# Kernel tuning notes

Measured on AMD Instinct MI355X. Metric: run time of the kernel, lower is better.

## Reference

```python
import jax, jax.numpy as jnp
import numpy as np

N, D, H, O = 2048, 128, 256, 1  # batch, input_dim, hidden_dim, output_dim
LN_EPS = 1e-5


def setup_inputs() -> dict:
    key = jax.random.key(0)
    ks = jax.random.split(key, 10)
    s = lambda fan_in: 1.0 / np.sqrt(fan_in)
    return {
        "array": jax.random.normal(ks[0], (N, D), dtype=jnp.float32),
        # per-feature Linear(1, H) stacked: weight [D, H], bias [D, H]
        "W_in": jax.random.uniform(ks[1], (D, H), jnp.float32, -1.0, 1.0),
        "b_in": jax.random.uniform(ks[2], (D, H), jnp.float32, -1.0, 1.0),
        # FactorAttentionLayer (width D): W: Linear(D, D), V: Linear(D, 1), LayerNorm(D)
        "Wf": jax.random.uniform(ks[3], (D, D), jnp.float32, -s(D), s(D)),
        "bf": jax.random.uniform(ks[4], (D,), jnp.float32, -s(D), s(D)),
        "Vf": jax.random.uniform(ks[5], (D,), jnp.float32, -s(D), s(D)),
        "bv": jnp.zeros((), jnp.float32),
        "ln_g": jnp.ones((D,), jnp.float32),
        "ln_b": jnp.zeros((D,), jnp.float32),
        # fc_hidden: Linear(D*H, H); fc_output: Linear(H, O)  (stored as [in, out])
        "Wh": jax.random.uniform(ks[6], (D * H, H), jnp.float32, -s(D * H), s(D * H)),
        "bh": jax.random.uniform(ks[7], (H,), jnp.float32, -s(D * H), s(D * H)),
        "Wo": jax.random.uniform(ks[8], (H, O), jnp.float32, -s(H), s(H)),
        "bo": jax.random.uniform(ks[9], (O,), jnp.float32, -s(H), s(H)),
    }


def reference(array, W_in, b_in, Wf, bf, Vf, bv, ln_g, ln_b, Wh, bh, Wo, bo):
    # Fused per-feature Linear(1,H)+ReLU: [n, D, H]
    p = jax.nn.relu(array[:, :, None] * W_in[None] + b_in[None])
    # permute(0, 2, 1) -> [n, H, D]
    x = jnp.transpose(p, (0, 2, 1))
    # FactorAttention: tanh-linear, softmax over axis 1 (the H axis), residual mul, LayerNorm over D
    u = jnp.tanh(jnp.einsum('nhd,de->nhe', x, Wf) + bf)          # [n, H, D]
    scores = jnp.einsum('nhd,d->nh', u, Vf) + bv                  # [n, H]
    attn = jax.nn.softmax(scores, axis=1)[:, :, None]             # [n, H, 1]
    y = x + x * attn                                              # [n, H, D]
    mu = jnp.mean(y, axis=-1, keepdims=True)
    var = jnp.mean((y - mu) ** 2, axis=-1, keepdims=True)
    y = (y - mu) * jax.lax.rsqrt(var + LN_EPS) * ln_g + ln_b
    # flatten [n, H*D] and MLP head (dropout = identity in eval)
    xx = y.reshape(y.shape[0], -1)
    h = jax.nn.relu(xx @ Wh + bh)
    return h @ Wo + bo
```

## Files before the change

### kernel.cpp

```cpp
#include <hip/hip_runtime.h>

#define NB 2048
#define DD 128
#define HH 256
#define KF 32768
#define LN_EPS 1e-5f

typedef __attribute__((ext_vector_type(8))) short short8;
typedef __attribute__((ext_vector_type(4))) float float4_t;

__device__ __forceinline__ unsigned short f2bf(float f) {
    unsigned int u = __builtin_bit_cast(unsigned int, f);
    u += 0x7fffu + ((u >> 16) & 1u);
    return (unsigned short)(u >> 16);
}

__device__ __forceinline__ void gl2lds16(const void* g, void* l) {
    __builtin_amdgcn_global_load_lds(
        (const __attribute__((address_space(1))) unsigned int*)g,
        (__attribute__((address_space(3))) unsigned int*)l, 16, 0, 0);
}

__global__ void prep_b(const float* __restrict__ Wh, unsigned short* __restrict__ WhbT) {
    __shared__ unsigned short tile[64][65];
    int kb = blockIdx.x;
    int jb = blockIdx.y;
    int t = threadIdx.x;
    int c = t & 63, r4 = t >> 6;
    int kap0 = kb * 64;
    int d  = kap0 >> 8;
    int h0 = kap0 & 255;
    for (int rr = r4; rr < 64; rr += 4) {
        int k = (h0 + rr) * 128 + d;
        tile[rr][c] = f2bf(Wh[(long)k * 256 + jb * 64 + c]);
    }
    __syncthreads();
    for (int rr = r4; rr < 64; rr += 4) {
        WhbT[(long)(jb * 64 + rr) * KF + kap0 + c] = tile[c][rr];
    }
}

__global__ void zgen(const float* __restrict__ arr, const float* __restrict__ Win,
                     const float* __restrict__ bin, const float* __restrict__ g,
                     const float* __restrict__ beta, unsigned short* __restrict__ Z) {
    __shared__ float a_s[4][128];
    __shared__ float g_s[128], b_s[128];
    int t = threadIdx.x;
    int n0 = blockIdx.x * 4;
    if (t < 128) { g_s[t] = g[t]; b_s[t] = beta[t]; }
    for (int i = t; i < 512; i += 256) a_s[i >> 7][i & 127] = arr[n0 * 128 + i];
    __syncthreads();
    int h = t;
    float sum[4] = {0.f, 0.f, 0.f, 0.f}, ssq[4] = {0.f, 0.f, 0.f, 0.f};
    for (int d = 0; d < 128; ++d) {
        float w = Win[d * 256 + h];
        float bb = bin[d * 256 + h];
#pragma unroll
        for (int q = 0; q < 4; ++q) {
            float x = fmaxf(fmaf(a_s[q][d], w, bb), 0.f);
            sum[q] += x; ssq[q] += x * x;
        }
    }
    float mu[4], rs[4];
#pragma unroll
    for (int q = 0; q < 4; ++q) {
        mu[q] = sum[q] * (1.f / 128.f);
        float var = fmaxf(ssq[q] * (1.f / 128.f) - mu[q] * mu[q], 0.f);
        rs[q] = rsqrtf(var + LN_EPS);
    }
    for (int d = 0; d < 128; ++d) {
        float w = Win[d * 256 + h];
        float bb = bin[d * 256 + h];
        float gg = g_s[d], be = b_s[d];
#pragma unroll
        for (int q = 0; q < 4; ++q) {
            float x = fmaxf(fmaf(a_s[q][d], w, bb), 0.f);
            float zv = fmaf((x - mu[q]) * rs[q], gg, be);
            Z[(long)(n0 + q) * KF + d * 256 + h] = f2bf(zv);
        }
    }
}

#define BM 128
#define BN 128
#define BK 32
#define KSPLIT 16
#define KSL (KF / KSPLIT)

__global__ __launch_bounds__(256, 2) void gemm_k(
        const unsigned short* __restrict__ A,
        const unsigned short* __restrict__ Bt,
        float* __restrict__ Cp) {
    __shared__ unsigned short As[BM * BK];
    __shared__ unsigned short Bs[BN * BK];
    int bid = blockIdx.x;
    int ks = bid >> 5;
    int mt = (bid >> 1) & 15;
    int nt = bid & 1;
    int m0 = mt * BM, n0 = nt * BN, k0 = ks * KSL;
    int t = threadIdx.x;
    int lane = t & 63, wave = t >> 6;
    int wm = (wave >> 1) * 64, wn = (wave & 1) * 64;
    int fr = lane & 15;
    int fk = (lane >> 4) * 8;

    float4_t acc[4][4] = {};

    const unsigned short* Aab = A + (long)m0 * KF + k0;
    const unsigned short* Bab = Bt + (long)n0 * KF + k0;
    int s0 = t, s1 = t + 256;
    long aoff0 = (long)(s0 >> 2) * KF + (long)(s0 & 3) * 8;
    long aoff1 = (long)(s1 >> 2) * KF + (long)(s1 & 3) * 8;

    for (int kk = 0; kk < KSL; kk += BK) {
        __syncthreads();
        gl2lds16(Aab + kk + aoff0, &As[s0 * 8]);
        gl2lds16(Aab + kk + aoff1, &As[s1 * 8]);
        gl2lds16(Bab + kk + aoff0, &Bs[s0 * 8]);
        gl2lds16(Bab + kk + aoff1, &Bs[s1 * 8]);
        __syncthreads();
        short8 af[4], bfv[4];
#pragma unroll
        for (int i = 0; i < 4; ++i)
            af[i] = *(const short8*)&As[(wm + i * 16 + fr) * BK + fk];
#pragma unroll
        for (int i = 0; i < 4; ++i)
            bfv[i] = *(const short8*)&Bs[(wn + i * 16 + fr) * BK + fk];
#pragma unroll
        for (int mi = 0; mi < 4; ++mi)
#pragma unroll
            for (int ni = 0; ni < 4; ++ni)
                acc[mi][ni] = __builtin_amdgcn_mfma_f32_16x16x32_bf16(
                    af[mi], bfv[ni], acc[mi][ni], 0, 0, 0);
    }

    int rb = (lane >> 4) * 4;
    float* Cb = Cp + (long)ks * NB * 256;
#pragma unroll
    for (int mi = 0; mi < 4; ++mi) {
#pragma unroll
        for (int ni = 0; ni < 4; ++ni) {
            int n = n0 + wn + ni * 16 + fr;
#pragma unroll
            for (int r = 0; r < 4; ++r) {
                int m = m0 + wm + mi * 16 + rb + r;
                Cb[(long)m * 256 + n] = acc[mi][ni][r];
            }
        }
    }
}

__global__ void finale(const float* __restrict__ Cp, const float* __restrict__ bh,
                       const float* __restrict__ Wo, const float* __restrict__ bo,
                       float* __restrict__ out) {
    __shared__ float red[4];
    int n = blockIdx.x, t = threadIdx.x;
    int lane = t & 63, wave = t >> 6;
    float s = bh[t];
    for (int sl = 0; sl < KSPLIT; ++sl)
        s += Cp[(long)sl * NB * 256 + (long)n * 256 + t];
    float v = fmaxf(s, 0.f) * Wo[t];
#pragma unroll
    for (int o = 32; o; o >>= 1) v += __shfl_down(v, o);
    if (lane == 0) red[wave] = v;
    __syncthreads();
    if (t == 0) out[n] = red[0] + red[1] + red[2] + red[3] + bo[0];
}

extern "C" void kernel_launch(void* const* d_in, const int* in_sizes, int n_in,
                              void* d_out, int out_size, void* d_ws, size_t ws_size,
                              hipStream_t stream) {
    const float* arr  = (const float*)d_in[0];
    const float* Win  = (const float*)d_in[1];
    const float* bin  = (const float*)d_in[2];
    const float* ln_g = (const float*)d_in[7];
    const float* ln_b = (const float*)d_in[8];
    const float* Wh   = (const float*)d_in[9];
    const float* bh   = (const float*)d_in[10];
    const float* Wo   = (const float*)d_in[11];
    const float* bo   = (const float*)d_in[12];
    float* out = (float*)d_out;

    char* ws = (char*)d_ws;
    unsigned short* WhbT = (unsigned short*)ws;
    unsigned short* Z    = (unsigned short*)(ws + 16777216ull);
    float* Cp            = (float*)(ws + 16777216ull + 134217728ull);

    hipLaunchKernelGGL(prep_b, dim3(512, 4), dim3(256), 0, stream, Wh, WhbT);
    hipLaunchKernelGGL(zgen, dim3(512), dim3(256), 0, stream, arr, Win, bin, ln_g, ln_b, Z);
    hipLaunchKernelGGL(gemm_k, dim3(512), dim3(256), 0, stream, Z, WhbT, Cp);
    hipLaunchKernelGGL(finale, dim3(NB), dim3(256), 0, stream, Cp, bh, Wo, bo, out);
}
```

Before: 207.8 us.

## Fuse LayerNorm activation generation into GEMM A-operand load, fold gamma/beta into weights

Instead of materializing the normalized bf16 activation matrix Z (about 128MB) in global memory, a stats kernel computes per-row LayerNorm mean and rstd. The GEMM then regenerates the relu(linear) values on the fly from the input, the transposed W_in/b_in and those stats, packing them to bf16 in registers as the MFMA A operand. LayerNorm gamma is folded into the bf16 Wh copy, and beta is folded into an extra bias vector that is accumulated with atomics and added in the final kernel. This removes the large Z write and read traffic. In exchange the GEMM does more ALU work per tile and makes scattered stats loads.

New measurement: 243.5 us. 17.2% more time.

```diff
diff --git a/kernel.cpp b/kernel.cpp
--- a/kernel.cpp
+++ b/kernel.cpp
@@ -5,9 +5,12 @@
 #define HH 256
 #define KF 32768
 #define LN_EPS 1e-5f
+#define KSPLIT 16
+#define KSL (KF / KSPLIT)
 
 typedef __attribute__((ext_vector_type(8))) short short8;
 typedef __attribute__((ext_vector_type(4))) float float4_t;
+typedef __attribute__((ext_vector_type(4))) float f4;
 
 __device__ __forceinline__ unsigned short f2bf(float f) {
     unsigned int u = __builtin_bit_cast(unsigned int, f);
@@ -15,39 +18,47 @@
     return (unsigned short)(u >> 16);
 }
 
+__device__ __forceinline__ unsigned int pkbf(float lo, float hi) {
+    unsigned int r;
+    asm("v_cvt_pk_bf16_f32 %0, %1, %2" : "=v"(r) : "v"(lo), "v"(hi));
+    return r;
+}
+
 __device__ __forceinline__ void gl2lds16(const void* g, void* l) {
     __builtin_amdgcn_global_load_lds(
         (const __attribute__((address_space(1))) unsigned int*)g,
         (__attribute__((address_space(3))) unsigned int*)l, 16, 0, 0);
 }
 
-__global__ void prep_b(const float* __restrict__ Wh, unsigned short* __restrict__ WhbT) {
-    __shared__ unsigned short tile[64][65];
-    int kb = blockIdx.x;
-    int jb = blockIdx.y;
+__global__ void stats_k(const float* __restrict__ arr, const float* __restrict__ Win,
+                        const float* __restrict__ bin, float2* __restrict__ stats,
+                        float* __restrict__ WinT, float* __restrict__ binT,
+                        float* __restrict__ bias2) {
+    __shared__ float a_s[4][128];
+    __shared__ float tile[32][33];
+    int bid = blockIdx.x;
     int t = threadIdx.x;
-    int c = t & 63, r4 = t >> 6;
-    int kap0 = kb * 64;
-    int d  = kap0 >> 8;
-    int h0 = kap0 & 255;
-    for (int rr = r4; rr < 64; rr += 4) {
-        int k = (h0 + rr) * 128 + d;
-        tile[rr][c] = f2bf(Wh[(long)k * 256 + jb * 64 + c]);
-    }
-    __syncthreads();
-    for (int rr = r4; rr < 64; rr += 4) {
-        WhbT[(long)(jb * 64 + rr) * KF + kap0 + c] = tile[c][rr];
-    }
-}
-
-__global__ void zgen(const float* __restrict__ arr, const float* __restrict__ Win,
-                     const float* __restrict__ bin, const float* __restrict__ g,
-                     const float* __restrict__ beta, unsigned short* __restrict__ Z) {
-    __shared__ float a_s[4][128];
-    __shared__ float g_s[128], b_s[128];
-    int t = threadIdx.x;
-    int n0 = blockIdx.x * 4;
-    if (t < 128) { g_s[t] = g[t]; b_s[t] = beta[t]; }
+
+    if (bid >= 512) {
+        if (bid == 576) { bias2[t & 255] = 0.f; return; }
+        int tid = bid - 512;
+        int mat = tid >> 5;
+        int dt = (tid >> 3) & 3;
+        int ht = tid & 7;
+        const float* src = mat ? bin : Win;
+        float* dst = mat ? binT : WinT;
+        int c = t & 31, r = t >> 5;
+#pragma unroll
+        for (int rr = r; rr < 32; rr += 8)
+            tile[rr][c] = src[(dt * 32 + rr) * 256 + ht * 32 + c];
+        __syncthreads();
+#pragma unroll
+        for (int rr = r; rr < 32; rr += 8)
+            dst[(ht * 32 + rr) * 128 + dt * 32 + c] = tile[c][rr];
+        return;
+    }
+
+    int n0 = bid * 4;
     for (int i = t; i < 512; i += 256) a_s[i >> 7][i & 127] = arr[n0 * 128 + i];
     __syncthreads();
     int h = t;
@@ -58,80 +69,123 @@
 #pragma unroll
         for (int q = 0; q < 4; ++q) {
             float x = fmaxf(fmaf(a_s[q][d], w, bb), 0.f);
-            sum[q] += x; ssq[q] += x * x;
-        }
-    }
-    float mu[4], rs[4];
+            sum[q] += x;
+            ssq[q] = fmaf(x, x, ssq[q]);
+        }
+    }
 #pragma unroll
     for (int q = 0; q < 4; ++q) {
-        mu[q] = sum[q] * (1.f / 128.f);
-        float var = fmaxf(ssq[q] * (1.f / 128.f) - mu[q] * mu[q], 0.f);
-        rs[q] = rsqrtf(var + LN_EPS);
-    }
-    for (int d = 0; d < 128; ++d) {
-        float w = Win[d * 256 + h];
-        float bb = bin[d * 256 + h];
-        float gg = g_s[d], be = b_s[d];
-#pragma unroll
-        for (int q = 0; q < 4; ++q) {
-            float x = fmaxf(fmaf(a_s[q][d], w, bb), 0.f);
-            float zv = fmaf((x - mu[q]) * rs[q], gg, be);
-            Z[(long)(n0 + q) * KF + d * 256 + h] = f2bf(zv);
-        }
-    }
-}
-
-#define BM 128
-#define BN 128
-#define BK 32
-#define KSPLIT 16
-#define KSL (KF / KSPLIT)
-
-__global__ __launch_bounds__(256, 2) void gemm_k(
-        const unsigned short* __restrict__ A,
+        float mu = sum[q] * (1.f / 128.f);
+        float var = fmaxf(ssq[q] * (1.f / 128.f) - mu * mu, 0.f);
+        float rs = rsqrtf(var + LN_EPS);
+        stats[(long)(n0 + q) * HH + h] = make_float2(rs, mu * rs);
+    }
+}
+
+__global__ void prep_b(const float* __restrict__ Wh, const float* __restrict__ g,
+                       const float* __restrict__ beta, unsigned short* __restrict__ WhbT,
+                       float* __restrict__ bias2) {
+    __shared__ unsigned short tile[64][65];
+    __shared__ float red[4][64];
+    int kb = blockIdx.x;
+    int jb = blockIdx.y;
+    int t = threadIdx.x;
+    int c = t & 63, r4 = t >> 6;
+    int k0 = kb * 64;
+    float bsum = 0.f;
+    for (int rr = r4; rr < 64; rr += 4) {
+        int k = k0 + rr, d = k & 127;
+        float v = Wh[(long)k * 256 + jb * 64 + c];
+        tile[rr][c] = f2bf(g[d] * v);
+        bsum = fmaf(beta[d], v, bsum);
+    }
+    __syncthreads();
+    for (int rr = r4; rr < 64; rr += 4)
+        WhbT[(long)(jb * 64 + rr) * KF + k0 + c] = tile[c][rr];
+    red[r4][c] = bsum;
+    __syncthreads();
+    if (r4 == 0)
+        atomicAdd(&bias2[jb * 64 + c], red[0][c] + red[1][c] + red[2][c] + red[3][c]);
+}
+
+__global__ __launch_bounds__(256, 2) void gemm_f(
+        const float* __restrict__ arr, const float* __restrict__ WinT,
+        const float* __restrict__ binT, const float2* __restrict__ stats,
         const unsigned short* __restrict__ Bt,
         float* __restrict__ Cp) {
-    __shared__ unsigned short As[BM * BK];
-    __shared__ unsigned short Bs[BN * BK];
+    __shared__ unsigned short Bs[128 * 32];
     int bid = blockIdx.x;
     int ks = bid >> 5;
     int mt = (bid >> 1) & 15;
     int nt = bid & 1;
-    int m0 = mt * BM, n0 = nt * BN, k0 = ks * KSL;
+    int m0 = mt * 128, n0 = nt * 128;
+    long k0 = (long)ks * KSL;
+    int h0 = ks * 16;
     int t = threadIdx.x;
     int lane = t & 63, wave = t >> 6;
     int wm = (wave >> 1) * 64, wn = (wave & 1) * 64;
     int fr = lane & 15;
-    int fk = (lane >> 4) * 8;
+    int fk8 = (lane >> 4) * 8;
 
     float4_t acc[4][4] = {};
 
-    const unsigned short* Aab = A + (long)m0 * KF + k0;
     const unsigned short* Bab = Bt + (long)n0 * KF + k0;
     int s0 = t, s1 = t + 256;
-    long aoff0 = (long)(s0 >> 2) * KF + (long)(s0 & 3) * 8;
-    long aoff1 = (long)(s1 >> 2) * KF + (long)(s1 & 3) * 8;
-
-    for (int kk = 0; kk < KSL; kk += BK) {
-        __syncthreads();
-        gl2lds16(Aab + kk + aoff0, &As[s0 * 8]);
-        gl2lds16(Aab + kk + aoff1, &As[s1 * 8]);
-        gl2lds16(Bab + kk + aoff0, &Bs[s0 * 8]);
-        gl2lds16(Bab + kk + aoff1, &Bs[s1 * 8]);
-        __syncthreads();
-        short8 af[4], bfv[4];
-#pragma unroll
-        for (int i = 0; i < 4; ++i)
-            af[i] = *(const short8*)&As[(wm + i * 16 + fr) * BK + fk];
-#pragma unroll
-        for (int i = 0; i < 4; ++i)
-            bfv[i] = *(const short8*)&Bs[(wn + i * 16 + fr) * BK + fk];
-#pragma unroll
-        for (int mi = 0; mi < 4; ++mi)
-#pragma unroll
-            for (int ni = 0; ni < 4; ++ni)
-                acc[mi][ni] = __builtin_amdgcn_mfma_f32_16x16x32_bf16(
-                    af[mi], bfv[ni], acc[mi][ni], 0, 0, 0);
+    long boff0 = (long)(s0 >> 2) * KF + (long)(s0 & 3) * 8;
+    long boff1 = (long)(s1 >> 2) * KF + (long)(s1 & 3) * 8;
+
+    int row0 = m0 + wm + fr;
+
+    for (int q = 0; q < 4; ++q) {
+        f4 a0[4], a1[4];
+#pragma unroll
+        for (int mi = 0; mi < 4; ++mi) {
+            const float* ap = arr + (long)(row0 + mi * 16) * DD + q * 32 + fk8;
+            a0[mi] = *(const f4*)ap;
+            a1[mi] = *(const f4*)(ap + 4);
+        }
+        for (int hl = 0; hl < 16; ++hl) {
+            int kb = hl * 128 + q * 32;
+            __syncthreads();
+            gl2lds16(Bab + kb + boff0, &Bs[s0 * 8]);
+            gl2lds16(Bab + kb + boff1, &Bs[s1 * 8]);
+            int h = h0 + hl;
+            const float* wp = WinT + h * DD + q * 32 + fk8;
+            const float* bp = binT + h * DD + q * 32 + fk8;
+            f4 w0 = *(const f4*)wp, w1 = *(const f4*)(wp + 4);
+            f4 v0 = *(const f4*)bp, v1 = *(const f4*)(bp + 4);
+            short8 af[4];
+#pragma unroll
+            for (int mi = 0; mi < 4; ++mi) {
+                float2 sv = stats[(long)(row0 + mi * 16) * HH + h];
+                float rs = sv.x, nm = -sv.y;
+                float z0 = fmaf(fmaxf(fmaf(a0[mi][0], w0[0], v0[0]), 0.f), rs, nm);
+                float z1 = fmaf(fmaxf(fmaf(a0[mi][1], w0[1], v0[1]), 0.f), rs, nm);
+                float z2 = fmaf(fmaxf(fmaf(a0[mi][2], w0[2], v0[2]), 0.f), rs, nm);
+                float z3 = fmaf(fmaxf(fmaf(a0[mi][3], w0[3], v0[3]), 0.f), rs, nm);
+                float z4 = fmaf(fmaxf(fmaf(a1[mi][0], w1[0], v1[0]), 0.f), rs, nm);
+                float z5 = fmaf(fmaxf(fmaf(a1[mi][1], w1[1], v1[1]), 0.f), rs, nm);
+                float z6 = fmaf(fmaxf(fmaf(a1[mi][2], w1[2], v1[2]), 0.f), rs, nm);
+                float z7 = fmaf(fmaxf(fmaf(a1[mi][3], w1[3], v1[3]), 0.f), rs, nm);
+                union { short8 s; unsigned int u[4]; } pk;
+                pk.u[0] = pkbf(z0, z1);
+                pk.u[1] = pkbf(z2, z3);
+                pk.u[2] = pkbf(z4, z5);
+                pk.u[3] = pkbf(z6, z7);
+                af[mi] = pk.s;
+            }
+            __syncthreads();
+            short8 bfv[4];
+#pragma unroll
+            for (int i = 0; i < 4; ++i)
+                bfv[i] = *(const short8*)&Bs[(wn + i * 16 + fr) * 32 + fk8];
+#pragma unroll
+            for (int mi = 0; mi < 4; ++mi)
+#pragma unroll
+                for (int ni = 0; ni < 4; ++ni)
+                    acc[mi][ni] = __builtin_amdgcn_mfma_f32_16x16x32_bf16(
+                        af[mi], bfv[ni], acc[mi][ni], 0, 0, 0);
+        }
     }
 
     int rb = (lane >> 4) * 4;
@@ -152,11 +206,11 @@
 
 __global__ void finale(const float* __restrict__ Cp, const float* __restrict__ bh,
                        const float* __restrict__ Wo, const float* __restrict__ bo,
-                       float* __restrict__ out) {
+                       const float* __restrict__ bias2, float* __restrict__ out) {
     __shared__ float red[4];
     int n = blockIdx.x, t = threadIdx.x;
     int lane = t & 63, wave = t >> 6;
-    float s = bh[t];
+    float s = bh[t] + bias2[t];
     for (int sl = 0; sl < KSPLIT; ++sl)
         s += Cp[(long)sl * NB * 256 + (long)n * 256 + t];
     float v = fmaxf(s, 0.f) * Wo[t];
@@ -183,11 +237,18 @@
 
     char* ws = (char*)d_ws;
     unsigned short* WhbT = (unsigned short*)ws;
-    unsigned short* Z    = (unsigned short*)(ws + 16777216ull);
-    float* Cp            = (float*)(ws + 16777216ull + 134217728ull);
-
-    hipLaunchKernelGGL(prep_b, dim3(512, 4), dim3(256), 0, stream, Wh, WhbT);
-    hipLaunchKernelGGL(zgen, dim3(512), dim3(256), 0, stream, arr, Win, bin, ln_g, ln_b, Z);
-    hipLaunchKernelGGL(gemm_k, dim3(512), dim3(256), 0, stream, Z, WhbT, Cp);
-    hipLaunchKernelGGL(finale, dim3(NB), dim3(256), 0, stream, Cp, bh, Wo, bo, out);
-}
+    float2* stats = (float2*)(ws + 16777216ull);
+    float* Cp     = (float*)(ws + 20971520ull);
+    float* WinT   = (float*)(ws + 54525952ull);
+    float* binT   = (float*)(ws + 54657024ull);
+    float* bias2  = (float*)(ws + 54788096ull);
+
+    hipLaunchKernelGGL(stats_k, dim3(577), dim3(256), 0, stream,
+                       arr, Win, bin, stats, WinT, binT, bias2);
+    hipLaunchKernelGGL(prep_b, dim3(512, 4), dim3(256), 0, stream,
+                       Wh, ln_g, ln_b, WhbT, bias2);
+    hipLaunchKernelGGL(gemm_f, dim3(512), dim3(256), 0, stream,
+                       arr, WinT, binT, stats, WhbT, Cp);
+    hipLaunchKernelGGL(finale, dim3(NB), dim3(256), 0, stream,
+                       Cp, bh, Wo, bo, bias2, out);
+}
```
